# Optimization experiments

Measured on AMD Instinct MI355X. Metric: run time of the kernel, lower is better.

Reference implementation:

```python
import jax, jax.numpy as jnp
import numpy as np

D_MODEL = 256
NUM_HEADS = 8
D_HEAD = D_MODEL // NUM_HEADS


def setup_inputs() -> dict:
    key = jax.random.key(0)
    ks = jax.random.split(key, 12)
    B, N, M, C = 1, 512, 512, D_MODEL
    s = 1.0 / np.sqrt(C)
    inp = {
        'input_q': jax.random.normal(ks[0], (B, N, C), jnp.float32),
        'input_k': jax.random.normal(ks[1], (B, M, C), jnp.float32),
        'input_v': jax.random.normal(ks[2], (B, M, C), jnp.float32),
        'embed_qk': jax.random.normal(ks[3], (B, N, M, C), jnp.float32),
        'Wq': jax.random.normal(ks[4], (C, C), jnp.float32) * s,
        'bq': jnp.zeros((C,), jnp.float32),
        'Wk': jax.random.normal(ks[5], (C, C), jnp.float32) * s,
        'bk': jnp.zeros((C,), jnp.float32),
        'Wv': jax.random.normal(ks[6], (C, C), jnp.float32) * s,
        'bv': jnp.zeros((C,), jnp.float32),
        'Wp': jax.random.normal(ks[7], (C, C), jnp.float32) * s,
        'bp': jnp.zeros((C,), jnp.float32),
    }
    return inp


def _split_heads(x, h):
    # (b, n, h*c) -> (b, h, n, c)
    b, n, _ = x.shape
    return x.reshape(b, n, h, -1).transpose(0, 2, 1, 3)


def reference(input_q, input_k, input_v, embed_qk, Wq, bq, Wk, bk, Wv, bv, Wp, bp):
    H = NUM_HEADS
    q = _split_heads(input_q @ Wq.T + bq, H)            # (b,h,n,c)
    k = _split_heads(input_k @ Wk.T + bk, H)            # (b,h,m,c)
    v = _split_heads(input_v @ Wv.T + bv, H)            # (b,h,m,c)
    p = embed_qk @ Wp.T + bp                            # (b,n,m,h*c)
    b_, n_, m_, _ = p.shape
    p = p.reshape(b_, n_, m_, H, -1).transpose(0, 3, 1, 2, 4)  # (b,h,n,m,c)
    scores_p = jnp.einsum('bhnc,bhnmc->bhnm', q, p)
    scores_e = jnp.einsum('bhnc,bhmc->bhnm', q, k)
    scores = (scores_e + scores_p) / jnp.sqrt(jnp.float32(D_HEAD))
    attn = jax.nn.softmax(scores, axis=-1)              # (b,h,n,m)
    hidden = jnp.einsum('bhnm,bhmc->bhnc', attn, v)
    b2, h2, n2, c2 = hidden.shape
    hidden = hidden.transpose(0, 2, 1, 3).reshape(b2, n2, h2 * c2)  # (b,n,C)
    return hidden, attn
```

## Files before the change

### kernel.cpp

```cpp
#include <hip/hip_runtime.h>
#include <math.h>

#define NN 512
#define CC 256
#define HH 8
#define DH 32

__global__ __launch_bounds__(512) void proj_kernel(
    const float* __restrict__ xq, const float* __restrict__ xk, const float* __restrict__ xv,
    const float* __restrict__ Wq, const float* __restrict__ bq,
    const float* __restrict__ Wk, const float* __restrict__ bk,
    const float* __restrict__ Wv, const float* __restrict__ bv,
    const float* __restrict__ Wp, const float* __restrict__ bp,
    float* __restrict__ qf, float* __restrict__ kf, float* __restrict__ vf,
    float* __restrict__ qw, float* __restrict__ qbp)
{
    __shared__ float x_lds[2][3][CC];
    __shared__ float q_lds[2][CC];
    const int t = threadIdx.x;
    const int n0 = blockIdx.x * 2;

    if (t < 384) {
        int hh = t / 192, rem = t % 192;
        int X = rem >> 6, c4 = (rem & 63) * 4;
        const float* xs = (X == 0) ? xq : (X == 1) ? xk : xv;
        *reinterpret_cast<float4*>(&x_lds[hh][X][c4]) =
            *reinterpret_cast<const float4*>(xs + (size_t)(n0 + hh) * CC + c4);
    }
    __syncthreads();

    const int half = t >> 8, j = t & 255;
    const int n = n0 + half;
    {
        float accq = 0.f, acck = 0.f, accv = 0.f;
        const float* wq = Wq + (size_t)j * CC;
        const float* wk = Wk + (size_t)j * CC;
        const float* wv = Wv + (size_t)j * CC;
        #pragma unroll 4
        for (int k4 = 0; k4 < CC / 4; ++k4) {
            float4 a = *reinterpret_cast<const float4*>(wq + k4 * 4);
            float4 b = *reinterpret_cast<const float4*>(wk + k4 * 4);
            float4 d = *reinterpret_cast<const float4*>(wv + k4 * 4);
            const float* x0 = &x_lds[half][0][k4 * 4];
            const float* x1 = &x_lds[half][1][k4 * 4];
            const float* x2 = &x_lds[half][2][k4 * 4];
            accq += x0[0]*a.x + x0[1]*a.y + x0[2]*a.z + x0[3]*a.w;
            acck += x1[0]*b.x + x1[1]*b.y + x1[2]*b.z + x1[3]*b.w;
            accv += x2[0]*d.x + x2[1]*d.y + x2[2]*d.z + x2[3]*d.w;
        }
        float vq = accq + bq[j];
        kf[(size_t)n * CC + j] = acck + bk[j];
        vf[(size_t)n * CC + j] = accv + bv[j];
        qf[(size_t)n * CC + j] = vq;
        q_lds[half][j] = vq;
    }
    __syncthreads();

    #pragma unroll
    for (int h = 0; h < HH; ++h) {
        float acc = 0.f;
        #pragma unroll 8
        for (int cc = 0; cc < DH; ++cc)
            acc += q_lds[half][h * DH + cc] * Wp[(size_t)(h * DH + cc) * CC + j];
        qw[((size_t)n * HH + h) * CC + j] = acc;
    }
    if (t < 16) {
        int hf = t >> 3, h = t & 7;
        float s = 0.f;
        for (int cc = 0; cc < DH; ++cc) s += q_lds[hf][h * DH + cc] * bp[h * DH + cc];
        qbp[(size_t)(n0 + hf) * HH + h] = s;
    }
}

__global__ __launch_bounds__(256) void escore_kernel(
    const float* __restrict__ qf, const float* __restrict__ kf, float* __restrict__ esc)
{
    const int b = blockIdx.x;
    const int h = b >> 6, nt = (b >> 3) & 7, mt = b & 7;
    const int n0 = nt * 64, m0 = mt * 64;
    const int t = threadIdx.x;

    __shared__ float q_t[64][33];
    __shared__ float k_t[64][33];

    #pragma unroll
    for (int it = 0; it < 2; ++it) {
        int idx = t + it * 256;
        int row = idx >> 3, c4 = (idx & 7) * 4;
        float4 qv = *reinterpret_cast<const float4*>(qf + (size_t)(n0 + row) * CC + h * DH + c4);
        float4 kv = *reinterpret_cast<const float4*>(kf + (size_t)(m0 + row) * CC + h * DH + c4);
        q_t[row][c4] = qv.x; q_t[row][c4+1] = qv.y; q_t[row][c4+2] = qv.z; q_t[row][c4+3] = qv.w;
        k_t[row][c4] = kv.x; k_t[row][c4+1] = kv.y; k_t[row][c4+2] = kv.z; k_t[row][c4+3] = kv.w;
    }
    __syncthreads();

    const int tx = t & 15, ty = t >> 4;
    float acc[4][4];
    #pragma unroll
    for (int i = 0; i < 4; ++i)
        #pragma unroll
        for (int jq = 0; jq < 4; ++jq) acc[i][jq] = 0.f;

    for (int cc = 0; cc < DH; ++cc) {
        float qa[4], kb[4];
        #pragma unroll
        for (int i = 0; i < 4; ++i) qa[i] = q_t[ty * 4 + i][cc];
        #pragma unroll
        for (int jq = 0; jq < 4; ++jq) kb[jq] = k_t[tx * 4 + jq][cc];
        #pragma unroll
        for (int i = 0; i < 4; ++i)
            #pragma unroll
            for (int jq = 0; jq < 4; ++jq) acc[i][jq] += qa[i] * kb[jq];
    }

    #pragma unroll
    for (int i = 0; i < 4; ++i) {
        float4 v = {acc[i][0], acc[i][1], acc[i][2], acc[i][3]};
        *reinterpret_cast<float4*>(esc + ((size_t)h * NN + n0 + ty * 4 + i) * NN + m0 + tx * 4) = v;
    }
}

__global__ __launch_bounds__(512, 2) void attn_kernel(
    const float* __restrict__ E, const float* __restrict__ qw,
    const float* __restrict__ qbp, const float* __restrict__ vf,
    float* __restrict__ attn_io, float* __restrict__ out_hidden)
{
    const int n = blockIdx.x;
    const int t = threadIdx.x;
    const int w = t >> 6, l = t & 63;
    const int r = l >> 4, c = l & 15;

    __shared__ float qw_lds[HH][CC];
    __shared__ float s_lds[HH][NN + 4];

    {
        float4 v = *reinterpret_cast<const float4*>(qw + (size_t)n * HH * CC + t * 4);
        reinterpret_cast<float4*>(qw_lds)[t] = v;
    }
    {
        const float* ep = attn_io + ((size_t)w * NN + n) * NN + l * 8;
        float4 a = *reinterpret_cast<const float4*>(ep);
        float4 b = *reinterpret_cast<const float4*>(ep + 4);
        *reinterpret_cast<float4*>(&s_lds[w][l * 8]) = a;
        *reinterpret_cast<float4*>(&s_lds[w][l * 8 + 4]) = b;
    }
    __syncthreads();

    const float* Ebase = E + (size_t)n * NN * CC;
    const int mbase = w * 64;

    #pragma unroll
    for (int g = 0; g < 4; ++g) {
        float acc[4][HH];
        #pragma unroll
        for (int it = 0; it < 4; ++it)
            #pragma unroll
            for (int h = 0; h < HH; ++h) acc[it][h] = 0.f;

        #pragma unroll
        for (int co = 0; co < 4; ++co) {
            const int o = co * 64 + c * 4;
            float4 e4[4];
            #pragma unroll
            for (int it = 0; it < 4; ++it)
                e4[it] = *reinterpret_cast<const float4*>(
                    Ebase + (size_t)(mbase + g * 16 + it * 4 + r) * CC + o);
            #pragma unroll
            for (int h = 0; h < HH; ++h) {
                float4 wv = *reinterpret_cast<const float4*>(&qw_lds[h][o]);
                #pragma unroll
                for (int it = 0; it < 4; ++it)
                    acc[it][h] += e4[it].x * wv.x + e4[it].y * wv.y +
                                  e4[it].z * wv.z + e4[it].w * wv.w;
            }
        }

        #pragma unroll
        for (int it = 0; it < 4; ++it) {
            float a0 = acc[it][0], a1 = acc[it][1], a2 = acc[it][2], a3 = acc[it][3];
            float a4 = acc[it][4], a5 = acc[it][5], a6 = acc[it][6], a7 = acc[it][7];
            const bool b1 = (c & 1), b2 = (c & 2), b4 = (c & 4);
            float t0 = b1 ? a0 : a4, t1 = b1 ? a1 : a5, t2 = b1 ? a2 : a6, t3 = b1 ? a3 : a7;
            float r0 = (b1 ? a4 : a0) + __shfl_xor(t0, 1);
            float r1 = (b1 ? a5 : a1) + __shfl_xor(t1, 1);
            float r2 = (b1 ? a6 : a2) + __shfl_xor(t2, 1);
            float r3 = (b1 ? a7 : a3) + __shfl_xor(t3, 1);
            t0 = b2 ? r0 : r2; t1 = b2 ? r1 : r3;
            float s0 = (b2 ? r2 : r0) + __shfl_xor(t0, 2);
            float s1 = (b2 ? r3 : r1) + __shfl_xor(t1, 2);
            t0 = b4 ? s0 : s1;
            float u0 = (b4 ? s1 : s0) + __shfl_xor(t0, 4);
            u0 += __shfl_xor(u0, 8);
            if (!(c & 8)) {
                int h = (c & 1) * 4 + (c & 2) + ((c >> 2) & 1);
                int row = mbase + g * 16 + it * 4 + r;
                s_lds[h][row] += u0;
            }
        }
    }
    __syncthreads();

    {
        const int h = w;
        const float qb = qbp[(size_t)n * HH + h];
        const float scale = 0.17677669529663687f;
        float vals[8];
        float mx = -1e30f;
        #pragma unroll
        for (int i = 0; i < 8; ++i) {
            vals[i] = (s_lds[h][l + i * 64] + qb) * scale;
            mx = fmaxf(mx, vals[i]);
        }
        #pragma unroll
        for (int off = 32; off > 0; off >>= 1) mx = fmaxf(mx, __shfl_xor(mx, off));
        float sum = 0.f;
        #pragma unroll
        for (int i = 0; i < 8; ++i) { vals[i] = __expf(vals[i] - mx); sum += vals[i]; }
        #pragma unroll
        for (int off = 32; off > 0; off >>= 1) sum += __shfl_xor(sum, off);
        float inv = 1.0f / sum;
        #pragma unroll
        for (int i = 0; i < 8; ++i) {
            float p = vals[i] * inv;
            int m = l + i * 64;
            s_lds[h][m] = p;
            attn_io[((size_t)h * NN + n) * NN + m] = p;
        }
    }
    __syncthreads();

    {
        float* part = &qw_lds[0][0];
        const int quad = t & 63;
        const int slice = w;
        const int h = quad >> 3;
        float4 a4 = {0.f, 0.f, 0.f, 0.f};
        const float* vb = vf + quad * 4;
        for (int mm = 0; mm < 64; ++mm) {
            int m = slice * 64 + mm;
            float a = s_lds[h][m];
            float4 vv = *reinterpret_cast<const float4*>(vb + (size_t)m * CC);
            a4.x += a * vv.x; a4.y += a * vv.y; a4.z += a * vv.z; a4.w += a * vv.w;
        }
        __syncthreads();
        *reinterpret_cast<float4*>(&part[slice * 256 + quad * 4]) = a4;
    }
    __syncthreads();
    if (t < 256) {
        const float* part = &qw_lds[0][0];
        float s = 0.f;
        #pragma unroll
        for (int sl = 0; sl < 8; ++sl) s += part[sl * 256 + t];
        out_hidden[(size_t)n * CC + t] = s;
    }
}

extern "C" void kernel_launch(void* const* d_in, const int* in_sizes, int n_in,
                              void* d_out, int out_size, void* d_ws, size_t ws_size,
                              hipStream_t stream) {
    const float* xq = (const float*)d_in[0];
    const float* xk = (const float*)d_in[1];
    const float* xv = (const float*)d_in[2];
    const float* E  = (const float*)d_in[3];
    const float* Wq = (const float*)d_in[4];
    const float* bq = (const float*)d_in[5];
    const float* Wk = (const float*)d_in[6];
    const float* bk = (const float*)d_in[7];
    const float* Wv = (const float*)d_in[8];
    const float* bv = (const float*)d_in[9];
    const float* Wp = (const float*)d_in[10];
    const float* bp = (const float*)d_in[11];

    float* ws = (float*)d_ws;
    float* qf  = ws;
    float* kf  = qf + NN * CC;
    float* vf  = kf + NN * CC;
    float* qw  = vf + NN * CC;
    float* qbp = qw + (size_t)NN * HH * CC;

    float* out_hidden = (float*)d_out;
    float* out_attn   = out_hidden + NN * CC;

    proj_kernel<<<NN / 2, 512, 0, stream>>>(xq, xk, xv, Wq, bq, Wk, bk, Wv, bv, Wp, bp,
                                            qf, kf, vf, qw, qbp);
    escore_kernel<<<512, 256, 0, stream>>>(qf, kf, out_attn);
    attn_kernel<<<NN, 512, 0, stream>>>(E, qw, qbp, vf, out_attn, out_hidden);
}
```

Baseline: 140.5 us.

## Fuse q·k score computation into attention kernel and double-buffer embed loads

Drops the separate escore kernel. Each attention block now computes its own q·k scores from qf/kf directly into shared memory, which removes one launch and the write and read-back of the score matrix through the attention output buffer. The embed_qk stream is software-pipelined with a two-stage register buffer using nontemporal loads, and the attention probabilities are written with nontemporal stores. In exchange, kf rows are re-read by every block, and the prefetch adds register pressure under the two-blocks-per-CU launch bound.

```diff
diff --git a/kernel.cpp b/kernel.cpp
--- a/kernel.cpp
+++ b/kernel.cpp
@@ -5,6 +5,8 @@
 #define CC 256
 #define HH 8
 #define DH 32
+
+typedef float vf4 __attribute__((ext_vector_type(4)));
 
 __global__ __launch_bounds__(512) void proj_kernel(
     const float* __restrict__ xq, const float* __restrict__ xk, const float* __restrict__ xv,
@@ -72,58 +74,28 @@
     }
 }
 
-__global__ __launch_bounds__(256) void escore_kernel(
-    const float* __restrict__ qf, const float* __restrict__ kf, float* __restrict__ esc)
-{
-    const int b = blockIdx.x;
-    const int h = b >> 6, nt = (b >> 3) & 7, mt = b & 7;
-    const int n0 = nt * 64, m0 = mt * 64;
-    const int t = threadIdx.x;
-
-    __shared__ float q_t[64][33];
-    __shared__ float k_t[64][33];
-
-    #pragma unroll
-    for (int it = 0; it < 2; ++it) {
-        int idx = t + it * 256;
-        int row = idx >> 3, c4 = (idx & 7) * 4;
-        float4 qv = *reinterpret_cast<const float4*>(qf + (size_t)(n0 + row) * CC + h * DH + c4);
-        float4 kv = *reinterpret_cast<const float4*>(kf + (size_t)(m0 + row) * CC + h * DH + c4);
-        q_t[row][c4] = qv.x; q_t[row][c4+1] = qv.y; q_t[row][c4+2] = qv.z; q_t[row][c4+3] = qv.w;
-        k_t[row][c4] = kv.x; k_t[row][c4+1] = kv.y; k_t[row][c4+2] = kv.z; k_t[row][c4+3] = kv.w;
-    }
-    __syncthreads();
-
-    const int tx = t & 15, ty = t >> 4;
-    float acc[4][4];
-    #pragma unroll
-    for (int i = 0; i < 4; ++i)
-        #pragma unroll
-        for (int jq = 0; jq < 4; ++jq) acc[i][jq] = 0.f;
-
-    for (int cc = 0; cc < DH; ++cc) {
-        float qa[4], kb[4];
-        #pragma unroll
-        for (int i = 0; i < 4; ++i) qa[i] = q_t[ty * 4 + i][cc];
-        #pragma unroll
-        for (int jq = 0; jq < 4; ++jq) kb[jq] = k_t[tx * 4 + jq][cc];
-        #pragma unroll
-        for (int i = 0; i < 4; ++i)
-            #pragma unroll
-            for (int jq = 0; jq < 4; ++jq) acc[i][jq] += qa[i] * kb[jq];
-    }
-
-    #pragma unroll
-    for (int i = 0; i < 4; ++i) {
-        float4 v = {acc[i][0], acc[i][1], acc[i][2], acc[i][3]};
-        *reinterpret_cast<float4*>(esc + ((size_t)h * NN + n0 + ty * 4 + i) * NN + m0 + tx * 4) = v;
-    }
+__device__ __forceinline__ float reduce8(const float a[HH], int c) {
+    const bool b1 = (c & 1), b2 = (c & 2), b4 = (c & 4);
+    float t0 = b1 ? a[0] : a[4], t1 = b1 ? a[1] : a[5],
+          t2 = b1 ? a[2] : a[6], t3 = b1 ? a[3] : a[7];
+    float r0 = (b1 ? a[4] : a[0]) + __shfl_xor(t0, 1);
+    float r1 = (b1 ? a[5] : a[1]) + __shfl_xor(t1, 1);
+    float r2 = (b1 ? a[6] : a[2]) + __shfl_xor(t2, 1);
+    float r3 = (b1 ? a[7] : a[3]) + __shfl_xor(t3, 1);
+    t0 = b2 ? r0 : r2; t1 = b2 ? r1 : r3;
+    float s0 = (b2 ? r2 : r0) + __shfl_xor(t0, 2);
+    float s1 = (b2 ? r3 : r1) + __shfl_xor(t1, 2);
+    t0 = b4 ? s0 : s1;
+    float u0 = (b4 ? s1 : s0) + __shfl_xor(t0, 4);
+    u0 += __shfl_xor(u0, 8);
+    return u0;
 }
 
 __global__ __launch_bounds__(512, 2) void attn_kernel(
-    const float* __restrict__ E, const float* __restrict__ qw,
-    const float* __restrict__ qbp, const float* __restrict__ vf,
-    float* __restrict__ attn_io, float* __restrict__ out_hidden)
+    const float* __restrict__ E, const float* __restrict__ qf,
+    const float* __restrict__ kf, const float* __restrict__ vf,
+    const float* __restrict__ qw, const float* __restrict__ qbp,
+    float* __restrict__ attn_out, float* __restrict__ out_hidden)
 {
     const int n = blockIdx.x;
     const int t = threadIdx.x;
@@ -137,64 +109,92 @@
         float4 v = *reinterpret_cast<const float4*>(qw + (size_t)n * HH * CC + t * 4);
         reinterpret_cast<float4*>(qw_lds)[t] = v;
     }
-    {
-        const float* ep = attn_io + ((size_t)w * NN + n) * NN + l * 8;
-        float4 a = *reinterpret_cast<const float4*>(ep);
-        float4 b = *reinterpret_cast<const float4*>(ep + 4);
-        *reinterpret_cast<float4*>(&s_lds[w][l * 8]) = a;
-        *reinterpret_cast<float4*>(&s_lds[w][l * 8 + 4]) = b;
-    }
-    __syncthreads();
+    __syncthreads();
+
+    const int mbase = w * 64;
+
+    {
+        float4 q4[4];
+        #pragma unroll
+        for (int co = 0; co < 4; ++co)
+            q4[co] = *reinterpret_cast<const float4*>(qf + (size_t)n * CC + co * 64 + c * 4);
+
+        for (int g = 0; g < 4; ++g) {
+            float acc[4][HH];
+            #pragma unroll
+            for (int it = 0; it < 4; ++it)
+                #pragma unroll
+                for (int h = 0; h < HH; ++h) acc[it][h] = 0.f;
+
+            #pragma unroll
+            for (int co = 0; co < 4; ++co) {
+                const int o = co * 64 + c * 4;
+                #pragma unroll
+                for (int it = 0; it < 4; ++it) {
+                    const int m = mbase + g * 16 + it * 4 + r;
+                    float4 k4 = *reinterpret_cast<const float4*>(kf + (size_t)m * CC + o);
+                    float kd = k4.x * q4[co].x + k4.y * q4[co].y +
+                               k4.z * q4[co].z + k4.w * q4[co].w;
+                    acc[it][2 * co    ] += (c & 8) ? 0.f : kd;
+                    acc[it][2 * co + 1] += (c & 8) ? kd : 0.f;
+                }
+            }
+            #pragma unroll
+            for (int it = 0; it < 4; ++it) {
+                float u0 = reduce8(acc[it], c);
+                if (!(c & 8)) {
+                    int h = (c & 1) * 4 + (c & 2) + ((c >> 2) & 1);
+                    s_lds[h][mbase + g * 16 + it * 4 + r] = u0;
+                }
+            }
+        }
+    }
 
     const float* Ebase = E + (size_t)n * NN * CC;
-    const int mbase = w * 64;
-
-    #pragma unroll
-    for (int g = 0; g < 4; ++g) {
-        float acc[4][HH];
+    {
+        vf4 ebuf[2][4];
         #pragma unroll
         for (int it = 0; it < 4; ++it)
-            #pragma unroll
-            for (int h = 0; h < HH; ++h) acc[it][h] = 0.f;
-
-        #pragma unroll
-        for (int co = 0; co < 4; ++co) {
-            const int o = co * 64 + c * 4;
-            float4 e4[4];
+            ebuf[0][it] = __builtin_nontemporal_load(reinterpret_cast<const vf4*>(
+                Ebase + (size_t)(mbase + it * 4 + r) * CC + c * 4));
+
+        for (int g = 0; g < 4; ++g) {
+            float acc[4][HH];
             #pragma unroll
             for (int it = 0; it < 4; ++it)
-                e4[it] = *reinterpret_cast<const float4*>(
-                    Ebase + (size_t)(mbase + g * 16 + it * 4 + r) * CC + o);
-            #pragma unroll
-            for (int h = 0; h < HH; ++h) {
-                float4 wv = *reinterpret_cast<const float4*>(&qw_lds[h][o]);
-                #pragma unroll
-                for (int it = 0; it < 4; ++it)
-                    acc[it][h] += e4[it].x * wv.x + e4[it].y * wv.y +
-                                  e4[it].z * wv.z + e4[it].w * wv.w;
-            }
-        }
-
-        #pragma unroll
-        for (int it = 0; it < 4; ++it) {
-            float a0 = acc[it][0], a1 = acc[it][1], a2 = acc[it][2], a3 = acc[it][3];
-            float a4 = acc[it][4], a5 = acc[it][5], a6 = acc[it][6], a7 = acc[it][7];
-            const bool b1 = (c & 1), b2 = (c & 2), b4 = (c & 4);
-            float t0 = b1 ? a0 : a4, t1 = b1 ? a1 : a5, t2 = b1 ? a2 : a6, t3 = b1 ? a3 : a7;
-            float r0 = (b1 ? a4 : a0) + __shfl_xor(t0, 1);
-            float r1 = (b1 ? a5 : a1) + __shfl_xor(t1, 1);
-            float r2 = (b1 ? a6 : a2) + __shfl_xor(t2, 1);
-            float r3 = (b1 ? a7 : a3) + __shfl_xor(t3, 1);
-            t0 = b2 ? r0 : r2; t1 = b2 ? r1 : r3;
-            float s0 = (b2 ? r2 : r0) + __shfl_xor(t0, 2);
-            float s1 = (b2 ? r3 : r1) + __shfl_xor(t1, 2);
-            t0 = b4 ? s0 : s1;
-            float u0 = (b4 ? s1 : s0) + __shfl_xor(t0, 4);
-            u0 += __shfl_xor(u0, 8);
-            if (!(c & 8)) {
-                int h = (c & 1) * 4 + (c & 2) + ((c >> 2) & 1);
-                int row = mbase + g * 16 + it * 4 + r;
-                s_lds[h][row] += u0;
+                #pragma unroll
+                for (int h = 0; h < HH; ++h) acc[it][h] = 0.f;
+
+            #pragma unroll
+            for (int co = 0; co < 4; ++co) {
+                const int cur = co & 1;
+                if (g < 3 || co < 3) {
+                    const int cn = (co + 1) & 3;
+                    const int gn = (co == 3) ? g + 1 : g;
+                    #pragma unroll
+                    for (int it = 0; it < 4; ++it)
+                        ebuf[cur ^ 1][it] = __builtin_nontemporal_load(
+                            reinterpret_cast<const vf4*>(
+                                Ebase + (size_t)(mbase + gn * 16 + it * 4 + r) * CC +
+                                cn * 64 + c * 4));
+                }
+                const int o = co * 64 + c * 4;
+                #pragma unroll
+                for (int h = 0; h < HH; ++h) {
+                    float4 wv = *reinterpret_cast<const float4*>(&qw_lds[h][o]);
+                    #pragma unroll
+                    for (int it = 0; it < 4; ++it)
+                        acc[it][h] += ebuf[cur][it][0] * wv.x + ebuf[cur][it][1] * wv.y +
+                                      ebuf[cur][it][2] * wv.z + ebuf[cur][it][3] * wv.w;
+                }
+            }
+            #pragma unroll
+            for (int it = 0; it < 4; ++it) {
+                float u0 = reduce8(acc[it], c);
+                if (!(c & 8)) {
+                    int h = (c & 1) * 4 + (c & 2) + ((c >> 2) & 1);
+                    s_lds[h][mbase + g * 16 + it * 4 + r] += u0;
+                }
             }
         }
     }
@@ -224,7 +224,7 @@
             float p = vals[i] * inv;
             int m = l + i * 64;
             s_lds[h][m] = p;
-            attn_io[((size_t)h * NN + n) * NN + m] = p;
+            __builtin_nontemporal_store(p, attn_out + ((size_t)h * NN + n) * NN + m);
         }
     }
     __syncthreads();
@@ -283,6 +283,5 @@
 
     proj_kernel<<<NN / 2, 512, 0, stream>>>(xq, xk, xv, Wq, bq, Wk, bk, Wv, bv, Wp, bp,
                                             qf, kf, vf, qw, qbp);
-    escore_kernel<<<512, 256, 0, stream>>>(qf, kf, out_attn);
-    attn_kernel<<<NN, 512, 0, stream>>>(E, qw, qbp, vf, out_attn, out_hidden);
-}
+    attn_kernel<<<NN, 512, 0, stream>>>(E, qf, kf, vf, qw, qbp, out_attn, out_hidden);
+}
```

After: 145.2 us. 3.4% more time.
